# Performance work log

Measured on AMD Instinct MI355X. Metric: run time of the kernel, lower is better.

Reference implementation:

```python
import jax, jax.numpy as jnp
import numpy as np

B, S, H = 16, 8192, 256


def setup_inputs() -> dict:
    key = jax.random.key(0)
    k1, k2, k3, k4, k5, k6 = jax.random.split(key, 6)
    # He/Glorot-ish scaling for the linear layer is irrelevant for correctness; use small randn.
    return {
        "query": jax.random.normal(k1, (B, 1, H), dtype=jnp.float32),
        "key": jax.random.normal(k2, (B, S, H), dtype=jnp.float32),
        "value": jax.random.normal(k3, (B, S, H), dtype=jnp.float32),
        "W_attn": jax.random.normal(k4, (H, 2 * H), dtype=jnp.float32) * 0.05,  # nn.Linear(2H, H).weight
        "b_attn": jax.random.normal(k5, (H,), dtype=jnp.float32) * 0.05,
        "v": jax.random.uniform(k6, (H,), dtype=jnp.float32),  # torch.rand init
    }


def reference(query, key, value, W_attn, b_attn, v):
    # Faithful to: tanh(Linear(cat([query.repeat(S), key], -1))) @ v -> softmax -> weighted sum.
    # Split the Linear weight so we never materialize the repeated/concatenated [B,S,2H] tensor:
    # cat([q,k]) @ W.T == q @ Wq.T + k @ Wk.T, with Wq = W[:, :H], Wk = W[:, H:].
    Wq = W_attn[:, :H]  # [H, H]
    Wk = W_attn[:, H:]  # [H, H]
    hidden = jnp.tanh(
        jnp.einsum("bqh,oh->bqo", query, Wq)        # [B,1,H], broadcasts over S
        + jnp.einsum("bsh,oh->bso", key, Wk)        # [B,S,H]
        + b_attn
    )  # [B,S,H]
    scores = jnp.einsum("bsh,h->bs", hidden, v)      # [B,S]
    attn_weights = jax.nn.softmax(scores, axis=-1)   # softmax over sequence
    context = jnp.einsum("bs,bsh->bh", attn_weights, value)[:, None, :]  # [B,1,H]
    return context, attn_weights
```

## Files before the change

### kernel.cpp

```cpp
#include <hip/hip_runtime.h>

#define B_SZ 16
#define S_SZ 8192
#define H_SZ 256

typedef _Float16 half8 __attribute__((ext_vector_type(8)));
typedef float f32x4 __attribute__((ext_vector_type(4)));

__device__ __forceinline__ float tanh_fast(float x) {
  float e = __expf(2.0f * x);
  return 1.0f - 2.0f / (e + 1.0f);
}

__device__ __forceinline__ unsigned map_f(float f) {
  unsigned u = __float_as_uint(f);
  return (u & 0x80000000u) ? ~u : (u | 0x80000000u);
}
__device__ __forceinline__ float unmap_f(unsigned u) {
  unsigned b = (u & 0x80000000u) ? (u ^ 0x80000000u) : ~u;
  return __uint_as_float(b);
}

__global__ __launch_bounds__(256) void prep_kernel(
    const float* __restrict__ query, const float* __restrict__ W_attn,
    const float* __restrict__ b_attn, float* __restrict__ qb,
    unsigned* __restrict__ mzu, float* __restrict__ Zf) {
  const int b = blockIdx.x;
  const int jo = blockIdx.y;
  const int wid = threadIdx.x >> 6;
  const int lane = threadIdx.x & 63;
  const float4 q4 = *(const float4*)(query + b * H_SZ + lane * 4);
#pragma unroll 4
  for (int i = 0; i < 16; i++) {
    const int o = jo * 64 + wid * 16 + i;
    const float4 w = *(const float4*)(W_attn + (size_t)o * 512 + lane * 4);
    float p = q4.x * w.x + q4.y * w.y + q4.z * w.z + q4.w * w.w;
#pragma unroll
    for (int off = 32; off >= 1; off >>= 1) p += __shfl_xor(p, off, 64);
    if (lane == 0) qb[b * H_SZ + o] = p + b_attn[o];
  }
  if (jo == 0 && threadIdx.x == 0) {
    mzu[b] = 0u;
    Zf[b] = 0.f;
  }
}

__global__ __launch_bounds__(1024, 4) void scores_kernel(
    const float* __restrict__ key, const float* __restrict__ W_attn,
    const float* __restrict__ qb, const float* __restrict__ vvec,
    float* __restrict__ scores, unsigned* __restrict__ mzu) {
  __shared__ _Float16 kbuf[2][32 * 256];
  __shared__ float psum[2][32];

  const int tid = threadIdx.x;
  const int wid = tid >> 6;
  const int lane = tid & 63;
  const int n = lane & 15;
  const int quad = lane >> 4;
  const int rowBase = blockIdx.x * 256;
  const int b = rowBase >> 13;

  half8 afrag[8];
  {
    const float* wrow = W_attn + (size_t)(wid * 16 + n) * 512 + 256 + quad * 8;
#pragma unroll
    for (int ks = 0; ks < 8; ks++) {
      float4 f0 = *(const float4*)(wrow + ks * 32);
      float4 f1 = *(const float4*)(wrow + ks * 32 + 4);
      half8 a;
      a[0] = (_Float16)f0.x; a[1] = (_Float16)f0.y;
      a[2] = (_Float16)f0.z; a[3] = (_Float16)f0.w;
      a[4] = (_Float16)f1.x; a[5] = (_Float16)f1.y;
      a[6] = (_Float16)f1.z; a[7] = (_Float16)f1.w;
      afrag[ks] = a;
    }
  }
  float qbv[4], vvv[4];
#pragma unroll
  for (int rg = 0; rg < 4; rg++) {
    qbv[rg] = qb[b * H_SZ + wid * 16 + quad * 4 + rg];
    vvv[rg] = vvec[wid * 16 + quad * 4 + rg];
  }

  if (tid < 64) ((float*)psum)[tid] = 0.f;

  const int srow = tid >> 5;
  const int sseg = tid & 31;
  const size_t sbase = (size_t)(rowBase + srow) * H_SZ + sseg * 8;
  const int sdst = srow * 256 + ((sseg ^ srow) << 3);

  {
    float4 f0 = *(const float4*)(key + sbase);
    float4 f1 = *(const float4*)(key + sbase + 4);
    half8 h;
    h[0] = (_Float16)f0.x; h[1] = (_Float16)f0.y;
    h[2] = (_Float16)f0.z; h[3] = (_Float16)f0.w;
    h[4] = (_Float16)f1.x; h[5] = (_Float16)f1.y;
    h[6] = (_Float16)f1.z; h[7] = (_Float16)f1.w;
    *(half8*)&kbuf[0][sdst] = h;
  }
  __syncthreads();

  float pmax = -1e30f;

  for (int c = 0; c < 8; c++) {
    float4 g0, g1;
    if (c < 7) {
      const size_t nb = sbase + (size_t)(c + 1) * 32 * H_SZ;
      g0 = *(const float4*)(key + nb);
      g1 = *(const float4*)(key + nb + 4);
    }
    const _Float16* kb = kbuf[c & 1];
#pragma unroll
    for (int rt = 0; rt < 2; rt++) {
      const int lrow = rt * 16 + n;
      f32x4 acc = {0.f, 0.f, 0.f, 0.f};
#pragma unroll
      for (int ks = 0; ks < 8; ks++) {
        half8 bfrag =
            *(const half8*)&kb[lrow * 256 + (((ks * 4 + quad) ^ lrow) << 3)];
        acc = __builtin_amdgcn_mfma_f32_16x16x32_f16(afrag[ks], bfrag, acc,
                                                     0, 0, 0);
      }
      float p = 0.f;
#pragma unroll
      for (int rg = 0; rg < 4; rg++)
        p = fmaf(vvv[rg], tanh_fast(qbv[rg] + acc[rg]), p);
      p += __shfl_xor(p, 16, 64);
      p += __shfl_xor(p, 32, 64);
      if (quad == 0) atomicAdd(&psum[c & 1][lrow], p);
    }
    if (c < 7) {
      half8 h;
      h[0] = (_Float16)g0.x; h[1] = (_Float16)g0.y;
      h[2] = (_Float16)g0.z; h[3] = (_Float16)g0.w;
      h[4] = (_Float16)g1.x; h[5] = (_Float16)g1.y;
      h[6] = (_Float16)g1.z; h[7] = (_Float16)g1.w;
      *(half8*)&kbuf[(c + 1) & 1][sdst] = h;
    }
    __syncthreads();
    if (tid < 32) {
      float val = psum[c & 1][tid];
      scores[rowBase + c * 32 + tid] = val;
      pmax = fmaxf(pmax, val);
      psum[c & 1][tid] = 0.f;
    }
  }
  if (wid == 0) {
#pragma unroll
    for (int off = 32; off >= 1; off >>= 1)
      pmax = fmaxf(pmax, __shfl_xor(pmax, off, 64));
    if (lane == 0) atomicMax(&mzu[b], map_f(pmax));
  }
}

__global__ __launch_bounds__(256) void reduce_kernel(
    const float* __restrict__ scores, const unsigned* __restrict__ mzu,
    float* __restrict__ Zf, float* __restrict__ ctx) {
  const int b = blockIdx.x >> 4;
  const int j = blockIdx.x & 15;
  const int tid = threadIdx.x;
  const float m = unmap_f(mzu[b]);
  const float* s = scores + b * S_SZ + j * 512;
  float part = __expf(s[tid] - m) + __expf(s[tid + 256] - m);
#pragma unroll
  for (int off = 32; off >= 1; off >>= 1) part += __shfl_xor(part, off, 64);
  __shared__ float red[4];
  if ((tid & 63) == 0) red[tid >> 6] = part;
  __syncthreads();
  if (tid == 0) atomicAdd(&Zf[b], red[0] + red[1] + red[2] + red[3]);
  if (tid < 16) ctx[b * H_SZ + j * 16 + tid] = 0.f;
}

__global__ __launch_bounds__(256) void context_kernel(
    const unsigned* __restrict__ mzu, const float* __restrict__ Zf,
    const float* __restrict__ value, float* __restrict__ attn,
    float* __restrict__ ctx) {
  __shared__ float wsm[256];
  __shared__ float4 psum4[3][64];
  const int b = blockIdx.x;
  const int j = blockIdx.y;
  const int t = threadIdx.x;
  const int g = t >> 6;
  const int hl = t & 63;
  const int s0 = j * 256;
  const float m = unmap_f(mzu[b]);
  const float invZ = 1.0f / Zf[b];
  float* arow = attn + b * S_SZ + s0;
  const float w = __expf(arow[t] - m) * invZ;
  arow[t] = w;
  wsm[t] = w;
  __syncthreads();
  const float4* vp =
      (const float4*)value + ((size_t)(b * S_SZ + s0 + g * 64)) * 64 + hl;
  float4 acc = {0.f, 0.f, 0.f, 0.f};
#pragma unroll 8
  for (int s = 0; s < 64; s++) {
    const float ww = wsm[g * 64 + s];
    const float4 vv = vp[(size_t)s * 64];
    acc.x = fmaf(ww, vv.x, acc.x);
    acc.y = fmaf(ww, vv.y, acc.y);
    acc.z = fmaf(ww, vv.z, acc.z);
    acc.w = fmaf(ww, vv.w, acc.w);
  }
  if (g > 0) psum4[g - 1][hl] = acc;
  __syncthreads();
  if (g == 0) {
    const float4 a1 = psum4[0][hl], a2 = psum4[1][hl], a3 = psum4[2][hl];
    acc.x += a1.x + a2.x + a3.x;
    acc.y += a1.y + a2.y + a3.y;
    acc.z += a1.z + a2.z + a3.z;
    acc.w += a1.w + a2.w + a3.w;
    float* cp = ctx + b * H_SZ + hl * 4;
    atomicAdd(cp + 0, acc.x);
    atomicAdd(cp + 1, acc.y);
    atomicAdd(cp + 2, acc.z);
    atomicAdd(cp + 3, acc.w);
  }
}

extern "C" void kernel_launch(void* const* d_in, const int* in_sizes, int n_in,
                              void* d_out, int out_size, void* d_ws,
                              size_t ws_size, hipStream_t stream) {
  const float* query = (const float*)d_in[0];
  const float* key = (const float*)d_in[1];
  const float* value = (const float*)d_in[2];
  const float* W_attn = (const float*)d_in[3];
  const float* b_attn = (const float*)d_in[4];
  const float* vvec = (const float*)d_in[5];

  float* out = (float*)d_out;
  float* ctx = out;
  float* attn = out + 4096;
  unsigned* mzu = (unsigned*)d_ws;
  float* Zf = (float*)d_ws + 16;

  prep_kernel<<<dim3(B_SZ, 4), 256, 0, stream>>>(query, W_attn, b_attn, ctx,
                                                 mzu, Zf);
  scores_kernel<<<512, 1024, 0, stream>>>(key, W_attn, ctx, vvec, attn, mzu);
  reduce_kernel<<<256, 256, 0, stream>>>(attn, mzu, Zf, ctx);
  context_kernel<<<dim3(B_SZ, 32), 256, 0, stream>>>(mzu, Zf, value, attn,
                                                     ctx);
}
```

Measured before the change: 324.7 us.

## Fuse softmax and value weighted sum into scores kernel with online softmax

The scores kernel now also reads the value rows for each 32-row chunk and accumulates a per-block partial context using an online softmax (running max and rescaled sum). A small combine kernel merges the 32 per-block partials per batch, writes the context, and normalizes the attention weights. This removes the separate reduce and context passes and the global atomic max/sum, so value is streamed while key is being processed. In exchange it adds per-chunk block-wide synchronization and serial softmax bookkeeping in one wave, plus extra register and LDS pressure from the value loads and the combine buffer.

```diff
diff --git a/kernel.cpp b/kernel.cpp
--- a/kernel.cpp
+++ b/kernel.cpp
@@ -12,19 +12,9 @@
   return 1.0f - 2.0f / (e + 1.0f);
 }
 
-__device__ __forceinline__ unsigned map_f(float f) {
-  unsigned u = __float_as_uint(f);
-  return (u & 0x80000000u) ? ~u : (u | 0x80000000u);
-}
-__device__ __forceinline__ float unmap_f(unsigned u) {
-  unsigned b = (u & 0x80000000u) ? (u ^ 0x80000000u) : ~u;
-  return __uint_as_float(b);
-}
-
 __global__ __launch_bounds__(256) void prep_kernel(
     const float* __restrict__ query, const float* __restrict__ W_attn,
-    const float* __restrict__ b_attn, float* __restrict__ qb,
-    unsigned* __restrict__ mzu, float* __restrict__ Zf) {
+    const float* __restrict__ b_attn, float* __restrict__ qb) {
   const int b = blockIdx.x;
   const int jo = blockIdx.y;
   const int wid = threadIdx.x >> 6;
@@ -39,18 +29,21 @@
     for (int off = 32; off >= 1; off >>= 1) p += __shfl_xor(p, off, 64);
     if (lane == 0) qb[b * H_SZ + o] = p + b_attn[o];
   }
-  if (jo == 0 && threadIdx.x == 0) {
-    mzu[b] = 0u;
-    Zf[b] = 0.f;
-  }
-}
-
-__global__ __launch_bounds__(1024, 4) void scores_kernel(
-    const float* __restrict__ key, const float* __restrict__ W_attn,
-    const float* __restrict__ qb, const float* __restrict__ vvec,
-    float* __restrict__ scores, unsigned* __restrict__ mzu) {
+}
+
+__global__ __launch_bounds__(1024, 4) void fused_kernel(
+    const float* __restrict__ key, const float* __restrict__ value,
+    const float* __restrict__ W_attn, const float* __restrict__ qb,
+    const float* __restrict__ vvec, float* __restrict__ scores,
+    float* __restrict__ ctxp, float* __restrict__ mblk,
+    float* __restrict__ zblk) {
   __shared__ _Float16 kbuf[2][32 * 256];
   __shared__ float psum[2][32];
+  __shared__ float warr[32];
+  __shared__ float msh;
+  __shared__ float zsh;
+  __shared__ float ssh;
+  __shared__ float4 comb[16][64];
 
   const int tid = threadIdx.x;
   const int wid = tid >> 6;
@@ -83,11 +76,17 @@
   }
 
   if (tid < 64) ((float*)psum)[tid] = 0.f;
+  if (tid == 0) {
+    msh = -1e30f;
+    zsh = 0.f;
+  }
 
   const int srow = tid >> 5;
   const int sseg = tid & 31;
   const size_t sbase = (size_t)(rowBase + srow) * H_SZ + sseg * 8;
   const int sdst = srow * 256 + ((sseg ^ srow) << 3);
+
+  const float* vbase = value + (size_t)(rowBase + 2 * wid) * H_SZ + lane * 4;
 
   {
     float4 f0 = *(const float4*)(key + sbase);
@@ -101,9 +100,11 @@
   }
   __syncthreads();
 
-  float pmax = -1e30f;
+  float4 acc4 = {0.f, 0.f, 0.f, 0.f};
 
   for (int c = 0; c < 8; c++) {
+    const float4 va = *(const float4*)(vbase + (size_t)c * 32 * H_SZ);
+    const float4 vb = *(const float4*)(vbase + (size_t)c * 32 * H_SZ + H_SZ);
     float4 g0, g1;
     if (c < 7) {
       const size_t nb = sbase + (size_t)(c + 1) * 32 * H_SZ;
@@ -139,83 +140,94 @@
       *(half8*)&kbuf[(c + 1) & 1][sdst] = h;
     }
     __syncthreads();
-    if (tid < 32) {
-      float val = psum[c & 1][tid];
-      scores[rowBase + c * 32 + tid] = val;
-      pmax = fmaxf(pmax, val);
-      psum[c & 1][tid] = 0.f;
-    }
-  }
-  if (wid == 0) {
-#pragma unroll
-    for (int off = 32; off >= 1; off >>= 1)
-      pmax = fmaxf(pmax, __shfl_xor(pmax, off, 64));
-    if (lane == 0) atomicMax(&mzu[b], map_f(pmax));
-  }
-}
-
-__global__ __launch_bounds__(256) void reduce_kernel(
-    const float* __restrict__ scores, const unsigned* __restrict__ mzu,
-    float* __restrict__ Zf, float* __restrict__ ctx) {
-  const int b = blockIdx.x >> 4;
-  const int j = blockIdx.x & 15;
-  const int tid = threadIdx.x;
-  const float m = unmap_f(mzu[b]);
-  const float* s = scores + b * S_SZ + j * 512;
-  float part = __expf(s[tid] - m) + __expf(s[tid + 256] - m);
-#pragma unroll
-  for (int off = 32; off >= 1; off >>= 1) part += __shfl_xor(part, off, 64);
-  __shared__ float red[4];
-  if ((tid & 63) == 0) red[tid >> 6] = part;
+
+    if (wid == 0) {
+      float s = (lane < 32) ? psum[c & 1][lane] : -1e30f;
+      if (lane < 32) {
+        scores[rowBase + c * 32 + lane] = s;
+        psum[c & 1][lane] = 0.f;
+      }
+      float cm = s;
+#pragma unroll
+      for (int off = 32; off >= 1; off >>= 1)
+        cm = fmaxf(cm, __shfl_xor(cm, off, 64));
+      const float m_old = msh;
+      const float m_new = fmaxf(m_old, cm);
+      const float scl = __expf(m_old - m_new);
+      float w = (lane < 32) ? __expf(s - m_new) : 0.f;
+      if (lane < 32) warr[lane] = w;
+      float zc = w;
+#pragma unroll
+      for (int off = 32; off >= 1; off >>= 1) zc += __shfl_xor(zc, off, 64);
+      if (lane == 0) {
+        msh = m_new;
+        zsh = fmaf(zsh, scl, zc);
+        ssh = scl;
+      }
+    }
+    __syncthreads();
+
+    const float scl = ssh;
+    const float w0 = warr[2 * wid];
+    const float w1 = warr[2 * wid + 1];
+    acc4.x = fmaf(w1, vb.x, fmaf(w0, va.x, acc4.x * scl));
+    acc4.y = fmaf(w1, vb.y, fmaf(w0, va.y, acc4.y * scl));
+    acc4.z = fmaf(w1, vb.z, fmaf(w0, va.z, acc4.z * scl));
+    acc4.w = fmaf(w1, vb.w, fmaf(w0, va.w, acc4.w * scl));
+  }
+
+  comb[wid][lane] = acc4;
   __syncthreads();
-  if (tid == 0) atomicAdd(&Zf[b], red[0] + red[1] + red[2] + red[3]);
-  if (tid < 16) ctx[b * H_SZ + j * 16 + tid] = 0.f;
-}
-
-__global__ __launch_bounds__(256) void context_kernel(
-    const unsigned* __restrict__ mzu, const float* __restrict__ Zf,
-    const float* __restrict__ value, float* __restrict__ attn,
+  if (tid < 64) {
+    float4 t4 = comb[0][tid];
+#pragma unroll
+    for (int j = 1; j < 16; j++) {
+      const float4 u = comb[j][tid];
+      t4.x += u.x; t4.y += u.y; t4.z += u.z; t4.w += u.w;
+    }
+    *(float4*)(ctxp + (size_t)blockIdx.x * 256 + tid * 4) = t4;
+  }
+  if (tid == 0) {
+    mblk[blockIdx.x] = msh;
+    zblk[blockIdx.x] = zsh;
+  }
+}
+
+__global__ __launch_bounds__(1024) void combine_kernel(
+    const float* __restrict__ ctxp, const float* __restrict__ mblk,
+    const float* __restrict__ zblk, float* __restrict__ attn,
     float* __restrict__ ctx) {
-  __shared__ float wsm[256];
-  __shared__ float4 psum4[3][64];
   const int b = blockIdx.x;
-  const int j = blockIdx.y;
   const int t = threadIdx.x;
-  const int g = t >> 6;
-  const int hl = t & 63;
-  const int s0 = j * 256;
-  const float m = unmap_f(mzu[b]);
-  const float invZ = 1.0f / Zf[b];
-  float* arow = attn + b * S_SZ + s0;
-  const float w = __expf(arow[t] - m) * invZ;
-  arow[t] = w;
-  wsm[t] = w;
+  __shared__ float ms[32], zs[32];
+  if (t < 32) {
+    ms[t] = mblk[b * 32 + t];
+    zs[t] = zblk[b * 32 + t];
+  }
   __syncthreads();
-  const float4* vp =
-      (const float4*)value + ((size_t)(b * S_SZ + s0 + g * 64)) * 64 + hl;
-  float4 acc = {0.f, 0.f, 0.f, 0.f};
-#pragma unroll 8
-  for (int s = 0; s < 64; s++) {
-    const float ww = wsm[g * 64 + s];
-    const float4 vv = vp[(size_t)s * 64];
-    acc.x = fmaf(ww, vv.x, acc.x);
-    acc.y = fmaf(ww, vv.y, acc.y);
-    acc.z = fmaf(ww, vv.z, acc.z);
-    acc.w = fmaf(ww, vv.w, acc.w);
-  }
-  if (g > 0) psum4[g - 1][hl] = acc;
-  __syncthreads();
-  if (g == 0) {
-    const float4 a1 = psum4[0][hl], a2 = psum4[1][hl], a3 = psum4[2][hl];
-    acc.x += a1.x + a2.x + a3.x;
-    acc.y += a1.y + a2.y + a3.y;
-    acc.z += a1.z + a2.z + a3.z;
-    acc.w += a1.w + a2.w + a3.w;
-    float* cp = ctx + b * H_SZ + hl * 4;
-    atomicAdd(cp + 0, acc.x);
-    atomicAdd(cp + 1, acc.y);
-    atomicAdd(cp + 2, acc.z);
-    atomicAdd(cp + 3, acc.w);
+  float m = -1e30f;
+#pragma unroll
+  for (int j = 0; j < 32; j++) m = fmaxf(m, ms[j]);
+  float Z = 0.f;
+  float e[32];
+#pragma unroll
+  for (int j = 0; j < 32; j++) {
+    e[j] = __expf(ms[j] - m);
+    Z = fmaf(zs[j], e[j], Z);
+  }
+  const float invZ = 1.0f / Z;
+  if (t < 256) {
+    float acc = 0.f;
+#pragma unroll
+    for (int j = 0; j < 32; j++)
+      acc = fmaf(ctxp[(size_t)(b * 32 + j) * 256 + t], e[j], acc);
+    ctx[b * H_SZ + t] = acc * invZ;
+  }
+  float* arow = attn + (size_t)b * S_SZ;
+#pragma unroll
+  for (int k = 0; k < 8; k++) {
+    const int idx = k * 1024 + t;
+    arow[idx] = __expf(arow[idx] - m) * invZ;
   }
 }
 
@@ -232,13 +244,12 @@
   float* out = (float*)d_out;
   float* ctx = out;
   float* attn = out + 4096;
-  unsigned* mzu = (unsigned*)d_ws;
-  float* Zf = (float*)d_ws + 16;
-
-  prep_kernel<<<dim3(B_SZ, 4), 256, 0, stream>>>(query, W_attn, b_attn, ctx,
-                                                 mzu, Zf);
-  scores_kernel<<<512, 1024, 0, stream>>>(key, W_attn, ctx, vvec, attn, mzu);
-  reduce_kernel<<<256, 256, 0, stream>>>(attn, mzu, Zf, ctx);
-  context_kernel<<<dim3(B_SZ, 32), 256, 0, stream>>>(mzu, Zf, value, attn,
-                                                     ctx);
-}
+  float* ctxp = (float*)d_ws;
+  float* mblk = ctxp + 512 * 256;
+  float* zblk = mblk + 512;
+
+  prep_kernel<<<dim3(B_SZ, 4), 256, 0, stream>>>(query, W_attn, b_attn, ctx);
+  fused_kernel<<<512, 1024, 0, stream>>>(key, value, W_attn, ctx, vvec, attn,
+                                         ctxp, mblk, zblk);
+  combine_kernel<<<B_SZ, 1024, 0, stream>>>(ctxp, mblk, zblk, attn, ctx);
+}
```

New measurement: 313.5 us. 3.4% less time.
